# Optimization experiments

Measured on AMD Instinct MI355X. Metric: run time of the kernel, lower is better.

## Reference

```python
import jax, jax.numpy as jnp
import numpy as np

TAU = 1.0
L = -0.1
R = 1.1
COUPLING_K = 2.0
EPS = 1e-6
LN_EPS = 1e-5


def entmax15(x, axis=-1):
    # Peters & Martins alpha=1.5 entmax via sort + threshold search.
    x = x / 2.0
    x = x - jnp.max(x, axis=axis, keepdims=True)
    xs = jnp.flip(jnp.sort(x, axis=axis), axis=axis)  # descending
    k = x.shape[axis]
    rho = jnp.arange(1, k + 1, dtype=x.dtype)
    mean = jnp.cumsum(xs, axis=axis) / rho
    mean_sq = jnp.cumsum(xs * xs, axis=axis) / rho
    ss = rho * (mean_sq - mean * mean)
    delta = jnp.clip((1.0 - ss) / rho, 0.0, None)
    tau = mean - jnp.sqrt(delta)
    support_size = jnp.sum(tau <= xs, axis=axis, keepdims=True)
    tau_star = jnp.take_along_axis(tau, support_size - 1, axis=axis)
    y = jnp.clip(x - tau_star, 0.0, None)
    return y * y


def setup_inputs() -> dict:
    key = jax.random.key(0)
    ks = jax.random.split(key, 4)
    B, S, D, H = 32, 4096, 768, 1024
    return {
        "embeddings": jax.random.normal(ks[0], (B, S, D), dtype=jnp.float32),
        "attn": jnp.ones((B, S), dtype=jnp.float32),
        "u": jax.random.uniform(ks[1], (B, S), dtype=jnp.float32),
        "ln_g": jnp.ones((D,), dtype=jnp.float32),
        "ln_b": jnp.zeros((D,), dtype=jnp.float32),
        "w1": jax.random.normal(ks[2], (H, D), dtype=jnp.float32) * 0.02,
        "b1": jnp.zeros((H,), dtype=jnp.float32),
        "w2": jax.random.normal(ks[3], (1, H), dtype=jnp.float32) * 0.02,
        "b2": jnp.zeros((1,), dtype=jnp.float32),
    }


def reference(embeddings, attn, u, ln_g, ln_b, w1, b1, w2, b2):
    # mask embeddings
    emb = embeddings * attn[..., None]                       # [B,S,D]
    # LayerNorm
    mu = jnp.mean(emb, axis=-1, keepdims=True)
    var = jnp.mean((emb - mu) ** 2, axis=-1, keepdims=True)
    x = (emb - mu) / jnp.sqrt(var + LN_EPS) * ln_g + ln_b
    # MLP scorer (dropout = identity in eval)
    h1 = jax.nn.gelu(jnp.einsum("bsd,hd->bsh", x, w1) + b1, approximate=False)
    scores = (jnp.einsum("bsh,oh->bso", h1, w2) + b2)[..., 0]  # [B,S]
    scores = jnp.where(attn == 0, -1e9, scores)
    # sparse attention over sequence axis
    z = entmax15(scores / TAU, axis=1) * attn
    # Kumaraswamy relaxed sampling with coupling
    eff = scores + COUPLING_K * (2.0 * z - 1.0)
    a = jax.nn.softplus(eff) + EPS
    b = jax.nn.softplus(-eff) + EPS
    uc = jnp.clip(u, EPS, 1.0 - EPS)
    xk = (1.0 - (1.0 - uc) ** (1.0 / b)) ** (1.0 / a)
    y = L + (R - L) * xk
    h = (jnp.clip(y, 0.0, 1.0) > 0.5).astype(scores.dtype) * attn
    # straight-through gate
    g = jax.lax.stop_gradient(h - z) + z
    reg = jnp.zeros((), dtype=scores.dtype)
    return (z, g, reg)
```

## Files before the change

kernel.cpp:

```cpp
#include <hip/hip_runtime.h>
#include <math.h>

#define NB 32
#define NS 4096
#define ND 768
#define NH 1024
#define NTOK (NB*NS)
#define NKC (ND/32)

typedef __bf16 bf16_t;
typedef __bf16 bf16x8 __attribute__((ext_vector_type(8)));
typedef float  f32x4  __attribute__((ext_vector_type(4)));

__global__ __launch_bounds__(256) void k_lnstats(
    const float* __restrict__ emb, const float* __restrict__ attn,
    float* __restrict__ mu_o, float* __restrict__ rs_o)
{
    const int token = blockIdx.x * 4 + (threadIdx.x >> 6);
    const int lane  = threadIdx.x & 63;
    const float am  = attn[token];
    const float* row = emb + (size_t)token * ND;

    float e[12];
    {
        const float4 v0 = *(const float4*)(row + lane * 4);
        const float4 v1 = *(const float4*)(row + 256 + lane * 4);
        const float4 v2 = *(const float4*)(row + 512 + lane * 4);
        e[0]=v0.x; e[1]=v0.y; e[2]=v0.z; e[3]=v0.w;
        e[4]=v1.x; e[5]=v1.y; e[6]=v1.z; e[7]=v1.w;
        e[8]=v2.x; e[9]=v2.y; e[10]=v2.z; e[11]=v2.w;
    }
    float s = 0.f;
#pragma unroll
    for (int j = 0; j < 12; j++) { e[j] *= am; s += e[j]; }
#pragma unroll
    for (int m = 32; m; m >>= 1) s += __shfl_xor(s, m, 64);
    const float mu = s * (1.0f / ND);

    float v = 0.f;
#pragma unroll
    for (int j = 0; j < 12; j++) { float d = e[j] - mu; v += d * d; }
#pragma unroll
    for (int m = 32; m; m >>= 1) v += __shfl_xor(v, m, 64);
    v *= (1.0f / ND);

    if (lane == 0) {
        mu_o[token] = mu;
        rs_o[token] = (float)(1.0 / sqrt((double)v + 1e-5));
    }
}

__global__ __launch_bounds__(256) void k_wprep(
    const float* __restrict__ w1, bf16_t* __restrict__ whB, bf16_t* __restrict__ wlB)
{
    const int t   = blockIdx.x * 256 + threadIdx.x;
    const int ln  = t & 63;
    const int h16 = (t >> 6) & 63;
    const int c   = t >> 12;
    const int row = h16 * 16 + (ln >> 2);
    const int k0  = c * 32 + 8 * ((ln & 3) ^ (ln >> 4));

    const float4 a = *(const float4*)(w1 + (size_t)row * ND + k0);
    const float4 b = *(const float4*)(w1 + (size_t)row * ND + k0 + 4);
    const float vv[8] = {a.x,a.y,a.z,a.w,b.x,b.y,b.z,b.w};
    bf16x8 hi, lo;
#pragma unroll
    for (int j = 0; j < 8; j++) {
        const bf16_t hj = (bf16_t)vv[j];
        hi[j] = hj;
        lo[j] = (bf16_t)(vv[j] - (float)hj);
    }
    const size_t o = (size_t)t * 8;
    *(bf16x8*)(whB + o) = hi;
    *(bf16x8*)(wlB + o) = lo;
}

#define TM 64
#define KC 32

__global__ __launch_bounds__(256, 2) void k_scorer(
    const float* __restrict__ emb, const float* __restrict__ attn,
    const float* __restrict__ ln_g, const float* __restrict__ ln_b,
    const bf16_t* __restrict__ whB, const bf16_t* __restrict__ wlB,
    const float* __restrict__ b1, const float* __restrict__ w2,
    const float* __restrict__ b2v,
    const float* __restrict__ mu_a, const float* __restrict__ rs_a,
    float* __restrict__ scores)
{
    __shared__ __align__(16) bf16_t sWh[512*32];
    __shared__ __align__(16) bf16_t sWl[512*32];
    __shared__ __align__(16) bf16_t sXh[64*32];
    __shared__ __align__(16) bf16_t sXl[64*32];
    __shared__ float sred[4*64];

    const int tid    = threadIdx.x;
    const int lane   = tid & 63;
    const int wv     = tid >> 6;
    const int token0 = blockIdx.x * TM;

    const int xt  = tid >> 2;
    const int xp  = tid & 3;
    const int xk8 = 8 * (xp ^ ((xt >> 2) & 3));
    const float x_mu = mu_a[token0 + xt];
    const float x_rs = rs_a[token0 + xt];
    const float x_at = attn[token0 + xt];
    const float* embrow = emb + (size_t)(token0 + xt) * ND;

    const int cn  = lane & 15;
    const int cq  = lane >> 4;
    const int fsw = (cq ^ (cn >> 2)) << 3;

    f32x4 acc[4][8];
    float spart[16];
#pragma unroll
    for (int i = 0; i < 16; i++) spart[i] = 0.f;

    for (int hh = 0; hh < 2; hh++) {
#pragma unroll
        for (int tt = 0; tt < 4; tt++)
#pragma unroll
            for (int ht = 0; ht < 8; ht++) acc[tt][ht] = (f32x4){0.f, 0.f, 0.f, 0.f};

        for (int kc = 0; kc < ND; kc += KC) {
            __syncthreads();
            {
                const size_t blk = ((size_t)((kc >> 5) * 64 + hh * 32 + wv * 8)) * 512 + lane * 8;
                const bf16_t* gh = whB + blk;
                const bf16_t* gl = wlB + blk;
#pragma unroll
                for (int i = 0; i < 8; i++)
                    __builtin_amdgcn_global_load_lds(
                        (const __attribute__((address_space(1))) void*)(gh + i * 512),
                        (__attribute__((address_space(3))) void*)&sWh[(wv*128 + i*16)*32],
                        16, 0, 0);
#pragma unroll
                for (int i = 0; i < 8; i++)
                    __builtin_amdgcn_global_load_lds(
                        (const __attribute__((address_space(1))) void*)(gl + i * 512),
                        (__attribute__((address_space(3))) void*)&sWl[(wv*128 + i*16)*32],
                        16, 0, 0);
            }
            {
                const float4 e0 = *(const float4*)(embrow + kc + xk8);
                const float4 e1 = *(const float4*)(embrow + kc + xk8 + 4);
                const float4 g0 = *(const float4*)(ln_g + kc + xk8);
                const float4 g1 = *(const float4*)(ln_g + kc + xk8 + 4);
                const float4 c0 = *(const float4*)(ln_b + kc + xk8);
                const float4 c1 = *(const float4*)(ln_b + kc + xk8 + 4);
                const float ev[8] = {e0.x,e0.y,e0.z,e0.w,e1.x,e1.y,e1.z,e1.w};
                const float gv[8] = {g0.x,g0.y,g0.z,g0.w,g1.x,g1.y,g1.z,g1.w};
                const float cv[8] = {c0.x,c0.y,c0.z,c0.w,c1.x,c1.y,c1.z,c1.w};
                bf16x8 hi, lo;
#pragma unroll
                for (int j = 0; j < 8; j++) {
                    const float x = (ev[j] * x_at - x_mu) * x_rs * gv[j] + cv[j];
                    const bf16_t hb = (bf16_t)x;
                    hi[j] = hb;
                    lo[j] = (bf16_t)(x - (float)hb);
                }
                *(bf16x8*)&sXh[xt*32 + xp*8] = hi;
                *(bf16x8*)&sXl[xt*32 + xp*8] = lo;
            }
            __syncthreads();
            bf16x8 ah[4], al[4];
#pragma unroll
            for (int tt = 0; tt < 4; tt++) {
                const int off = (tt*16 + cn)*32 + fsw;
                ah[tt] = *(const bf16x8*)&sXh[off];
                al[tt] = *(const bf16x8*)&sXl[off];
            }
#pragma unroll
            for (int ht = 0; ht < 8; ht++) {
                const int off = (wv*128 + ht*16 + cn)*32 + fsw;
                const bf16x8 bh = *(const bf16x8*)&sWh[off];
                const bf16x8 bl = *(const bf16x8*)&sWl[off];
#pragma unroll
                for (int tt = 0; tt < 4; tt++) {
                    acc[tt][ht] = __builtin_amdgcn_mfma_f32_16x16x32_bf16(ah[tt], bh, acc[tt][ht], 0, 0, 0);
                    acc[tt][ht] = __builtin_amdgcn_mfma_f32_16x16x32_bf16(al[tt], bh, acc[tt][ht], 0, 0, 0);
                    acc[tt][ht] = __builtin_amdgcn_mfma_f32_16x16x32_bf16(ah[tt], bl, acc[tt][ht], 0, 0, 0);
                }
            }
        }
#pragma unroll
        for (int ht = 0; ht < 8; ht++) {
            const int hg = hh*512 + wv*128 + ht*16 + cn;
            const float b1v = b1[hg];
            const float w2v = w2[hg];
#pragma unroll
            for (int tt = 0; tt < 4; tt++)
#pragma unroll
                for (int r = 0; r < 4; r++) {
                    const float pre = acc[tt][ht][r] + b1v;
                    const float ge  = 0.5f * pre * (1.0f + erff(pre * 0.70710678118654752f));
                    spart[tt*4 + r] += ge * w2v;
                }
        }
    }
#pragma unroll
    for (int i = 0; i < 16; i++) {
        float s = spart[i];
        s += __shfl_xor(s, 1, 64);
        s += __shfl_xor(s, 2, 64);
        s += __shfl_xor(s, 4, 64);
        s += __shfl_xor(s, 8, 64);
        spart[i] = s;
    }
    if (cn == 0) {
#pragma unroll
        for (int tt = 0; tt < 4; tt++)
#pragma unroll
            for (int r = 0; r < 4; r++)
                sred[wv*64 + tt*16 + cq*4 + r] = spart[tt*4 + r];
    }
    __syncthreads();
    if (tid < TM) {
        scores[token0 + tid] = sred[tid] + sred[64 + tid] + sred[128 + tid] + sred[192 + tid] + b2v[0];
    }
}

__global__ __launch_bounds__(1024) void k_tau(
    const float* __restrict__ scores, const float* __restrict__ attn,
    double* __restrict__ tau_o, double* __restrict__ mx_o)
{
    const int b    = blockIdx.x;
    const int tid  = threadIdx.x;
    const int lane = tid & 63;
    const int wid  = tid >> 6;

    __shared__ double redd[2][16];
    __shared__ float  redf[16];
    __shared__ float  bcf;

    float vv[4];
#pragma unroll
    for (int j = 0; j < 4; j++) {
        const int i = tid + 1024 * j;
        const float at = attn[b * NS + i];
        const float s  = scores[b * NS + i];
        vv[j] = ((at == 0.0f) ? -1e9f : s) * 0.5f;
    }

    float mx = fmaxf(fmaxf(vv[0], vv[1]), fmaxf(vv[2], vv[3]));
#pragma unroll
    for (int m = 32; m; m >>= 1) mx = fmaxf(mx, __shfl_xor(mx, m, 64));
    if (lane == 0) redf[wid] = mx;
    __syncthreads();
    if (tid == 0) {
        float t = redf[0];
        for (int i = 1; i < 16; i++) t = fmaxf(t, redf[i]);
        bcf = t;
    }
    __syncthreads();
    const double mxd = (double)bcf;

    double d[4];
#pragma unroll
    for (int j = 0; j < 4; j++) d[j] = (double)vv[j] - mxd;

    double lo = -1.0, hi = 0.0;
    for (int it = 0; it < 44; it++) {
        const double mid = 0.5 * (lo + hi);
        double s = 0.0;
#pragma unroll
        for (int j = 0; j < 4; j++) {
            const double t = d[j] - mid;
            if (t > 0.0) s += t * t;
        }
#pragma unroll
        for (int m = 32; m; m >>= 1) s += __shfl_xor(s, m, 64);
        const int p = it & 1;
        if (lane == 0) redd[p][wid] = s;
        __syncthreads();
        double tot = 0.0;
#pragma unroll
        for (int i = 0; i < 16; i++) tot += redd[p][i];
        if (tot >= 1.0) lo = mid; else hi = mid;
    }
    if (tid == 0) { tau_o[b] = lo; mx_o[b] = mxd; }
}

static __device__ __forceinline__ double softplus_d(double x) {
    return (x > 30.0) ? x : log1p(exp(x));
}

__global__ __launch_bounds__(256) void k_gate(
    const float* __restrict__ scores, const float* __restrict__ attn,
    const float* __restrict__ u,
    const double* __restrict__ tau_a, const double* __restrict__ mx_a,
    float* __restrict__ out)
{
    const int i0 = (blockIdx.x * 256 + threadIdx.x) * 4;
    const int b  = i0 >> 12;
    const double tau = tau_a[b];
    const double mxd = mx_a[b];

    const float4 s4 = *(const float4*)(scores + i0);
    const float4 a4 = *(const float4*)(attn + i0);
    const float4 u4 = *(const float4*)(u + i0);
    const float sv[4] = {s4.x, s4.y, s4.z, s4.w};
    const float av[4] = {a4.x, a4.y, a4.z, a4.w};
    const float uv[4] = {u4.x, u4.y, u4.z, u4.w};

    float zo[4], go[4];
#pragma unroll
    for (int j = 0; j < 4; j++) {
        const float at = av[j];
        const float sm = (at == 0.0f) ? -1e9f : sv[j];
        const float vvf = sm * 0.5f;
        const double dd = (double)vvf - mxd;
        const double t  = dd - tau;
        const double zz = (t > 0.0) ? t * t : 0.0;
        const float  z  = (float)zz * at;

        const double eff  = (double)sm + 2.0 * (2.0 * (double)z - 1.0);
        const double sp_p = softplus_d(eff)  + 1e-6;
        const double sp_n = softplus_d(-eff) + 1e-6;
        const double uc   = fmin(fmax((double)uv[j], 1e-6), 1.0 - 1e-6);
        const double xk   = pow(1.0 - pow(1.0 - uc, 1.0 / sp_n), 1.0 / sp_p);
        const double y    = -0.1 + 1.2 * xk;
        const double ycl  = fmin(fmax(y, 0.0), 1.0);
        float h = (ycl > 0.5) ? 1.0f : 0.0f;
        h *= at;
        zo[j] = z;
        go[j] = (h - z) + z;
    }
    *(float4*)(out + i0)        = (float4){zo[0], zo[1], zo[2], zo[3]};
    *(float4*)(out + NTOK + i0) = (float4){go[0], go[1], go[2], go[3]};
    if (i0 == 0) out[2 * NTOK] = 0.0f;
}

extern "C" void kernel_launch(void* const* d_in, const int* in_sizes, int n_in,
                              void* d_out, int out_size, void* d_ws, size_t ws_size,
                              hipStream_t stream)
{
    const float* emb  = (const float*)d_in[0];
    const float* attn = (const float*)d_in[1];
    const float* u    = (const float*)d_in[2];
    const float* ln_g = (const float*)d_in[3];
    const float* ln_b = (const float*)d_in[4];
    const float* w1   = (const float*)d_in[5];
    const float* b1   = (const float*)d_in[6];
    const float* w2   = (const float*)d_in[7];
    const float* b2   = (const float*)d_in[8];
    float* out = (float*)d_out;

    float*  wsf    = (float*)d_ws;
    float*  scores = wsf;
    float*  mu     = wsf + NTOK;
    float*  rs     = wsf + 2 * NTOK;
    double* taud   = (double*)(wsf + 3 * NTOK);
    double* mxd    = taud + NB;
    bf16_t* w1hB   = (bf16_t*)(mxd + NB);
    bf16_t* w1lB   = w1hB + (size_t)NH * ND;

    hipLaunchKernelGGL(k_lnstats, dim3(NTOK / 4), dim3(256), 0, stream,
                       emb, attn, mu, rs);
    hipLaunchKernelGGL(k_wprep, dim3((NKC * 64 * 64) / 256), dim3(256), 0, stream,
                       w1, w1hB, w1lB);
    hipLaunchKernelGGL(k_scorer, dim3(NTOK / TM), dim3(256), 0, stream,
                       emb, attn, ln_g, ln_b, w1hB, w1lB, b1, w2, b2, mu, rs, scores);
    hipLaunchKernelGGL(k_tau, dim3(NB), dim3(1024), 0, stream,
                       scores, attn, taud, mxd);
    hipLaunchKernelGGL(k_gate, dim3(NTOK / 1024), dim3(256), 0, stream,
                       scores, attn, u, taud, mxd, out);
}
```

Measured before the change: 1.532 ms.

## Shrink scorer H-tile to 256 and fuse tau search with gate kernel

```diff
diff --git a/kernel.cpp b/kernel.cpp
--- a/kernel.cpp
+++ b/kernel.cpp
@@ -87,8 +87,8 @@
     const float* __restrict__ mu_a, const float* __restrict__ rs_a,
     float* __restrict__ scores)
 {
-    __shared__ __align__(16) bf16_t sWh[512*32];
-    __shared__ __align__(16) bf16_t sWl[512*32];
+    __shared__ __align__(16) bf16_t sWh[256*32];
+    __shared__ __align__(16) bf16_t sWl[256*32];
     __shared__ __align__(16) bf16_t sXh[64*32];
     __shared__ __align__(16) bf16_t sXl[64*32];
     __shared__ float sred[4*64];
@@ -110,34 +110,34 @@
     const int cq  = lane >> 4;
     const int fsw = (cq ^ (cn >> 2)) << 3;
 
-    f32x4 acc[4][8];
+    f32x4 acc[4][4];
     float spart[16];
 #pragma unroll
     for (int i = 0; i < 16; i++) spart[i] = 0.f;
 
-    for (int hh = 0; hh < 2; hh++) {
+    for (int hq = 0; hq < 4; hq++) {
 #pragma unroll
         for (int tt = 0; tt < 4; tt++)
 #pragma unroll
-            for (int ht = 0; ht < 8; ht++) acc[tt][ht] = (f32x4){0.f, 0.f, 0.f, 0.f};
+            for (int ht = 0; ht < 4; ht++) acc[tt][ht] = (f32x4){0.f, 0.f, 0.f, 0.f};
 
         for (int kc = 0; kc < ND; kc += KC) {
             __syncthreads();
             {
-                const size_t blk = ((size_t)((kc >> 5) * 64 + hh * 32 + wv * 8)) * 512 + lane * 8;
+                const size_t blk = ((size_t)((kc >> 5) * 64 + hq * 16 + wv * 4)) * 512 + lane * 8;
                 const bf16_t* gh = whB + blk;
                 const bf16_t* gl = wlB + blk;
 #pragma unroll
-                for (int i = 0; i < 8; i++)
+                for (int i = 0; i < 4; i++)
                     __builtin_amdgcn_global_load_lds(
                         (const __attribute__((address_space(1))) void*)(gh + i * 512),
-                        (__attribute__((address_space(3))) void*)&sWh[(wv*128 + i*16)*32],
+                        (__attribute__((address_space(3))) void*)&sWh[(wv*64 + i*16)*32],
                         16, 0, 0);
 #pragma unroll
-                for (int i = 0; i < 8; i++)
+                for (int i = 0; i < 4; i++)
                     __builtin_amdgcn_global_load_lds(
                         (const __attribute__((address_space(1))) void*)(gl + i * 512),
-                        (__attribute__((address_space(3))) void*)&sWl[(wv*128 + i*16)*32],
+                        (__attribute__((address_space(3))) void*)&sWl[(wv*64 + i*16)*32],
                         16, 0, 0);
             }
             {
@@ -170,8 +170,8 @@
                 al[tt] = *(const bf16x8*)&sXl[off];
             }
 #pragma unroll
-            for (int ht = 0; ht < 8; ht++) {
-                const int off = (wv*128 + ht*16 + cn)*32 + fsw;
+            for (int ht = 0; ht < 4; ht++) {
+                const int off = (wv*64 + ht*16 + cn)*32 + fsw;
                 const bf16x8 bh = *(const bf16x8*)&sWh[off];
                 const bf16x8 bl = *(const bf16x8*)&sWl[off];
 #pragma unroll
@@ -183,8 +183,8 @@
             }
         }
 #pragma unroll
-        for (int ht = 0; ht < 8; ht++) {
-            const int hg = hh*512 + wv*128 + ht*16 + cn;
+        for (int ht = 0; ht < 4; ht++) {
+            const int hg = hq*256 + wv*64 + ht*16 + cn;
             const float b1v = b1[hg];
             const float w2v = w2[hg];
 #pragma unroll
@@ -219,9 +219,13 @@
     }
 }
 
-__global__ __launch_bounds__(1024) void k_tau(
+static __device__ __forceinline__ double softplus_d(double x) {
+    return (x > 30.0) ? x : log1p(exp(x));
+}
+
+__global__ __launch_bounds__(1024) void k_taugate(
     const float* __restrict__ scores, const float* __restrict__ attn,
-    double* __restrict__ tau_o, double* __restrict__ mx_o)
+    const float* __restrict__ u, float* __restrict__ out)
 {
     const int b    = blockIdx.x;
     const int tid  = threadIdx.x;
@@ -232,13 +236,14 @@
     __shared__ float  redf[16];
     __shared__ float  bcf;
 
-    float vv[4];
+    float vv[4], at[4], sm[4];
 #pragma unroll
     for (int j = 0; j < 4; j++) {
         const int i = tid + 1024 * j;
-        const float at = attn[b * NS + i];
-        const float s  = scores[b * NS + i];
-        vv[j] = ((at == 0.0f) ? -1e9f : s) * 0.5f;
+        at[j] = attn[b * NS + i];
+        const float s = scores[b * NS + i];
+        sm[j] = (at[j] == 0.0f) ? -1e9f : s;
+        vv[j] = sm[j] * 0.5f;
     }
 
     float mx = fmaxf(fmaxf(vv[0], vv[1]), fmaxf(vv[2], vv[3]));
@@ -277,57 +282,31 @@
         for (int i = 0; i < 16; i++) tot += redd[p][i];
         if (tot >= 1.0) lo = mid; else hi = mid;
     }
-    if (tid == 0) { tau_o[b] = lo; mx_o[b] = mxd; }
-}
-
-static __device__ __forceinline__ double softplus_d(double x) {
-    return (x > 30.0) ? x : log1p(exp(x));
-}
-
-__global__ __launch_bounds__(256) void k_gate(
-    const float* __restrict__ scores, const float* __restrict__ attn,
-    const float* __restrict__ u,
-    const double* __restrict__ tau_a, const double* __restrict__ mx_a,
-    float* __restrict__ out)
-{
-    const int i0 = (blockIdx.x * 256 + threadIdx.x) * 4;
-    const int b  = i0 >> 12;
-    const double tau = tau_a[b];
-    const double mxd = mx_a[b];
-
-    const float4 s4 = *(const float4*)(scores + i0);
-    const float4 a4 = *(const float4*)(attn + i0);
-    const float4 u4 = *(const float4*)(u + i0);
-    const float sv[4] = {s4.x, s4.y, s4.z, s4.w};
-    const float av[4] = {a4.x, a4.y, a4.z, a4.w};
-    const float uv[4] = {u4.x, u4.y, u4.z, u4.w};
-
-    float zo[4], go[4];
+    const double tau = lo;
+
+    if (b == 0 && tid == 0) out[2 * NTOK] = 0.0f;
+
 #pragma unroll
     for (int j = 0; j < 4; j++) {
-        const float at = av[j];
-        const float sm = (at == 0.0f) ? -1e9f : sv[j];
-        const float vvf = sm * 0.5f;
-        const double dd = (double)vvf - mxd;
-        const double t  = dd - tau;
+        const int i = tid + 1024 * j;
+        const double t  = d[j] - tau;
         const double zz = (t > 0.0) ? t * t : 0.0;
-        const float  z  = (float)zz * at;
-
-        const double eff  = (double)sm + 2.0 * (2.0 * (double)z - 1.0);
+        const float  z  = (float)zz * at[j];
+
+        const double eff  = (double)sm[j] + 2.0 * (2.0 * (double)z - 1.0);
         const double sp_p = softplus_d(eff)  + 1e-6;
         const double sp_n = softplus_d(-eff) + 1e-6;
-        const double uc   = fmin(fmax((double)uv[j], 1e-6), 1.0 - 1e-6);
+        const double uc   = fmin(fmax((double)u[b * NS + i], 1e-6), 1.0 - 1e-6);
         const double xk   = pow(1.0 - pow(1.0 - uc, 1.0 / sp_n), 1.0 / sp_p);
         const double y    = -0.1 + 1.2 * xk;
         const double ycl  = fmin(fmax(y, 0.0), 1.0);
         float h = (ycl > 0.5) ? 1.0f : 0.0f;
-        h *= at;
-        zo[j] = z;
-        go[j] = (h - z) + z;
-    }
-    *(float4*)(out + i0)        = (float4){zo[0], zo[1], zo[2], zo[3]};
-    *(float4*)(out + NTOK + i0) = (float4){go[0], go[1], go[2], go[3]};
-    if (i0 == 0) out[2 * NTOK] = 0.0f;
+        h *= at[j];
+        const float g = (h - z) + z;
+
+        out[b * NS + i]        = z;
+        out[NTOK + b * NS + i] = g;
+    }
 }
 
 extern "C" void kernel_launch(void* const* d_in, const int* in_sizes, int n_in,
@@ -349,9 +328,7 @@
     float*  scores = wsf;
     float*  mu     = wsf + NTOK;
     float*  rs     = wsf + 2 * NTOK;
-    double* taud   = (double*)(wsf + 3 * NTOK);
-    double* mxd    = taud + NB;
-    bf16_t* w1hB   = (bf16_t*)(mxd + NB);
+    bf16_t* w1hB   = (bf16_t*)(wsf + 3 * NTOK);
     bf16_t* w1lB   = w1hB + (size_t)NH * ND;
 
     hipLaunchKernelGGL(k_lnstats, dim3(NTOK / 4), dim3(256), 0, stream,
@@ -360,8 +337,6 @@
                        w1, w1hB, w1lB);
     hipLaunchKernelGGL(k_scorer, dim3(NTOK / TM), dim3(256), 0, stream,
                        emb, attn, ln_g, ln_b, w1hB, w1lB, b1, w2, b2, mu, rs, scores);
-    hipLaunchKernelGGL(k_tau, dim3(NB), dim3(1024), 0, stream,
-                       scores, attn, taud, mxd);
-    hipLaunchKernelGGL(k_gate, dim3(NTOK / 1024), dim3(256), 0, stream,
-                       scores, attn, u, taud, mxd, out);
-}
+    hipLaunchKernelGGL(k_taugate, dim3(NB), dim3(1024), 0, stream,
+                       scores, attn, u, out);
+}
```

New measurement: 1.362 ms. 11.1% less time.
